# Performance work log

Measured on AMD Instinct MI355X. Metric: run time of the kernel, lower is better.

The kernel has to match this reference:

```python
import jax, jax.numpy as jnp
import numpy as np

DEPTH = 10
LEAF = 2 ** DEPTH          # 1024 leaves
NODE_NUM = 2 * LEAF - 1    # 2047
N = NODE_NUM + 1           # 2048 nodes incl. global node 0
ATTN = 4
D = 128
B = 8
L = 2


def _trace_children(ni):
    terms = []
    s, e = ni << 1, (ni << 1) | 1
    while s <= NODE_NUM and e <= NODE_NUM:
        terms.extend(range(s, e + 1))
        s <<= 1
        e = (e << 1) | 1
    return terms


def _trace_left(si):
    ni, cd, terms, stop = si + LEAF, DEPTH, [], False
    while not stop:
        cs = ni - ATTN + 1 - ((ni - ATTN + 1) & 1)
        stop = cs < 2 ** cd
        cs = max(2 ** cd, cs)
        terms.extend(range(cs, ni + 1))
        ni = (cs - 1) >> 1
        cd -= 1
    return terms


def _trace_right(ei):
    ni, cd, terms, stop = ei + LEAF, DEPTH, [], False
    while not stop:
        ce = ni + ATTN - 1 + ((ni - ATTN) & 1)
        stop = ce >= 2 ** (cd + 1)
        ce = min(2 ** (cd + 1) - 1, ce)
        terms.extend(range(ni, ce + 1))
        ni = (ce + 1) >> 1
        cd -= 1
    return terms


def _build_edges():
    src, dst = [], []
    for ni in range(1, NODE_NUM + 1):
        if ni < LEAF:
            t = _trace_children(ni)
        else:
            t = _trace_left(ni - LEAF) + _trace_right(ni - LEAF)
        src.extend(t)
        dst.extend([ni] * len(t))
    e = np.stack([np.asarray(src, np.int64), np.asarray(dst, np.int64)])  # [2, E]
    off = np.arange(B, dtype=np.int64) * N
    eb = (e[:, None, :] + off[None, :, None]).reshape(2, -1)  # batch-offset like _fetch_edge_data
    return eb.astype(np.int32)


def setup_inputs() -> dict:
    key = jax.random.key(0)
    k0, k1, k2 = jax.random.split(key, 3)
    s = 1.0 / np.sqrt(D)
    return {
        "elements": jax.random.normal(k0, (B, LEAF, D), jnp.float32),
        "ln_gamma": jnp.ones((L, D), jnp.float32),
        "ln_beta": jnp.zeros((L, D), jnp.float32),
        "w_nei": (jax.random.normal(k1, (L, D, D), jnp.float32) * s),
        "b_nei": jnp.zeros((L, D), jnp.float32),
        "w_root": (jax.random.normal(k2, (L, D, D), jnp.float32) * s),
        "edge_index": jnp.asarray(_build_edges()),
    }


def _sinusoid(pos, d):
    # ArbitraryPositionEncoder: sinusoidal encoding over (possibly negative) positions
    half = d // 2
    inv = jnp.exp(-jnp.arange(half, dtype=jnp.float32) * (np.log(10000.0) / half))
    ang = pos[:, None] * inv[None, :]  # [n, half]
    return jnp.stack([jnp.sin(ang), jnp.cos(ang)], -1).reshape(pos.shape[0], d)


def reference(elements, ln_gamma, ln_beta, w_nei, b_nei, w_root, edge_index):
    Bx, leaf, d = elements.shape
    depth = int(np.log2(leaf))
    # bottom-up tree compression (mean of two children)
    cur = elements
    levels = [cur]
    for _ in range(depth):
        cur = 0.5 * (cur[:, 0::2] + cur[:, 1::2])
        levels.append(cur)
    # node ordering: [global node 0 (=-1), root (level 0), ..., leaves (level depth)]
    node_feat = jnp.concatenate(
        [jnp.full((Bx, 1, d), -1.0, elements.dtype)] + levels[::-1], axis=1)  # [B, N, D]
    n = node_feat.shape[1]
    # positional encoding: vertical = floor(log2(idx)), horizontal = idx - 2^vertical
    idx = jnp.arange(n, dtype=jnp.float32)
    vpos = jnp.floor(jnp.log2(jnp.where(idx == 0, 0.5, idx)))
    hpos = idx - jnp.exp2(vpos)
    enc = jnp.concatenate([_sinusoid(hpos, d // 2), _sinusoid(vpos, d // 2)], -1)  # [N, D]
    x = (node_feat + enc[None]).reshape(Bx * n, d)
    src, dst = edge_index[0], edge_index[1]
    nseg = Bx * n
    deg = jnp.maximum(
        jax.ops.segment_sum(jnp.ones(src.shape, jnp.float32), dst, num_segments=nseg), 1.0)
    # DeepGCNLayer res+ blocks with SAGEConv (mean aggr)
    for l in range(ln_gamma.shape[0]):
        mu = jnp.mean(x, -1, keepdims=True)
        var = jnp.mean((x - mu) ** 2, -1, keepdims=True)
        h = (x - mu) * jax.lax.rsqrt(var + 1e-5) * ln_gamma[l] + ln_beta[l]
        h = jax.nn.gelu(h, approximate=False)
        agg = jax.ops.segment_sum(h[src], dst, num_segments=nseg) / deg[:, None]
        h = agg @ w_nei[l] + b_nei[l] + h @ w_root[l]
        x = x + h
    return x.reshape(Bx, n, d)
```

## Files before the change

kernel.cpp:

```cpp
#include <hip/hip_runtime.h>
#include <hip/hip_bf16.h>

#define LEAFN 1024
#define NN    2048
#define BATCH 8
#define DD    128
#define ROWS  (BATCH*NN)
#define AHS   384
#define NB    256
#define NT    1024

#define LOG1E4_OVER_32 0.28782313662425575f

#define SLACK 9
#define CSTRIDE 136
#define SB_OFF   0
#define SBT      520
#define S_OFF    33280
#define SSTR     232
#define DEG_OFF  48128
#define FB_OFF   48256
#define AGGL_OFF 54672
#define RED_OFF  63376
#define RED2_OFF 64400

typedef __bf16 bf16x8 __attribute__((ext_vector_type(8)));
typedef float  floatx4 __attribute__((ext_vector_type(4)));
typedef float  floatx2 __attribute__((ext_vector_type(2)));

__device__ __forceinline__ float bf2f(unsigned short u) {
  return __uint_as_float(((unsigned)u) << 16);
}
__device__ __forceinline__ unsigned short f2bf(float f) {
  unsigned u = __float_as_uint(f);
  u += 0x7FFFu + ((u >> 16) & 1u);
  return (unsigned short)(u >> 16);
}
__device__ __forceinline__ float gelu(float v) {
  return 0.5f * v * (1.0f + erff(v * 0.70710678118f));
}
__device__ __forceinline__ floatx2 bfpair(unsigned u) {
  floatx2 r;
  r[0] = __uint_as_float(u << 16);
  r[1] = __uint_as_float(u & 0xffff0000u);
  return r;
}

__device__ __forceinline__ float enc_val(int node, int d) {
  float hp, vp;
  if (node == 0) { hp = -0.5f; vp = -1.0f; }
  else {
    int v = 31 - __clz(node);
    hp = (float)(node - (1 << v));
    vp = (float)v;
  }
  float pos = (d < 64) ? hp : vp;
  int i = ((d < 64) ? d : (d - 64)) >> 1;
  float inv = __expf(-(float)i * LOG1E4_OVER_32);
  float ang = pos * inv;
  return (d & 1) ? __cosf(ang) : __sinf(ang);
}

__device__ __forceinline__ void win_cd(int jb, int cd, int& lo_, int& wd_) {
  int g0 = 1024 + jb * 32, g1 = g0 + 31;
  int a0 = g0 >> (10 - cd), a1 = g1 >> (10 - cd);
  int l = a0 - SLACK, h = a1 + SLACK;
  int lvlo = 1 << cd, lvhi = (2 << cd) - 1;
  lo_ = l < lvlo ? lvlo : l;
  int hh = h > lvhi ? lvhi : h;
  int w = hh - lo_ + 1;
  wd_ = w < 0 ? 0 : w;
}

__device__ __forceinline__ void gbarN(int* bar, int slot) {
  __syncthreads();
  if (threadIdx.x == 0) {
    int g = blockIdx.x & 7;
    int* base = bar + (slot * 8 + g) * 64;
    __threadfence();
    if (__hip_atomic_fetch_add(base, 1, __ATOMIC_RELAXED,
                               __HIP_MEMORY_SCOPE_AGENT) == 31)
      __hip_atomic_store(base + 32, 1, __ATOMIC_RELAXED,
                         __HIP_MEMORY_SCOPE_AGENT);
    while (!__hip_atomic_load(base + 32, __ATOMIC_RELAXED,
                              __HIP_MEMORY_SCOPE_AGENT))
      __builtin_amdgcn_s_sleep(1);
    __threadfence();
  }
  __syncthreads();
}

__device__ __forceinline__ void ph_tree(char* smemc, int b, int s,
                                        const float* __restrict__ elements,
                                        float* __restrict__ x,
                                        float* __restrict__ lvl4,
                                        unsigned short* __restrict__ ah,
                                        const float* __restrict__ gamma,
                                        const float* __restrict__ beta,
                                        float* __restrict__ sroot,
                                        float* xci, int* bar) {
  float* sm = (float*)smemc;
  floatx4* smv = (floatx4*)smemc;
  int tid = threadIdx.x;
  const float4* src = (const float4*)(elements + (size_t)(b * LEAFN + s * 64) * DD);
  for (int i = tid; i < 2048; i += NT) {
    int f = i * 4;
    int j = f >> 7, d = f & 127;
    *(float4*)&sm[(63 + j) * DD + d] = src[i];
  }
  __syncthreads();
  for (int lv = 5; lv >= 0; --lv) {
    int nodes = 1 << lv;
    for (int idx = tid; idx < nodes * 32; idx += NT) {
      int k = nodes + (idx >> 5);
      int j = idx & 31;
      smv[(k - 1) * 32 + j] = 0.5f * (smv[(2 * k - 1) * 32 + j] + smv[(2 * k) * 32 + j]);
    }
    __syncthreads();
  }
  if (tid < 32) ((floatx4*)&lvl4[(size_t)(b * 16 + s) * DD])[tid] = smv[tid];
  __syncthreads();
  if (tid == 0) {
    __threadfence();
    __hip_atomic_store(bar + 1536 + b * 64 + s * 4, 1, __ATOMIC_RELAXED,
                       __HIP_MEMORY_SCOPE_AGENT);
  }
  {
    int d2 = tid & 63;
    int i = d2 & 31;
    float inv = __expf(-(float)i * LOG1E4_OVER_32);
    bool lowhalf = d2 < 32;
    for (int idx2 = tid; idx2 < 127 * 64; idx2 += NT) {
      int row = idx2 >> 6;
      int k = row + 1;
      int lv = 31 - __clz(k);
      int g = ((16 + s) << lv) | (k - (1 << lv));
      float vp = (float)(lv + 4);
      float hp = (float)(g - (16 << lv));
      float pos = lowhalf ? hp : vp;
      float sv, cv;
      __sincosf(pos * inv, &sv, &cv);
      int base = row * DD + 2 * d2;
      float xv0 = sm[base] + sv;
      float xv1 = sm[base + 1] + cv;
      sm[base] = xv0; sm[base + 1] = xv1;
      if (k >= 64 || k <= 32) {
        float2 o = make_float2(xv0, xv1);
        *(float2*)&x[((size_t)(b * NN + g)) * DD + 2 * d2] = o;
      }
    }
  }
  __syncthreads();
  {
    int wave = tid >> 6, lane = tid & 63;
    if (wave >= 8) {
      int wl = wave & 7;
      int mt = wl >> 2, nq = wl & 3;
      int m = lane & 15, q = lane >> 4;
#pragma unroll
      for (int ci = 0; ci < 2; ++ci)
#pragma unroll
        for (int r = 0; r < 4; ++r) {
          int t = 32 + mt * 16 + q * 4 + r;
          int k = (t == 63) ? 1 : t + 1;
          int d = (nq * 2 + ci) * 16 + m;
          xci[ci * 4 + r] = sm[(k - 1) * DD + d];
        }
    }
  }
  __syncthreads();
  {
    int sub = tid & 7, dp = sub * 16;
    for (int rr = tid >> 3; rr < 127; rr += NT / 8) {
      float* rowp = &sm[rr * DD + dp];
      float4 q0 = *(float4*)rowp;
      float4 q1 = *(float4*)(rowp + 4);
      float4 q2 = *(float4*)(rowp + 8);
      float4 q3 = *(float4*)(rowp + 12);
      float v[16] = {q0.x, q0.y, q0.z, q0.w, q1.x, q1.y, q1.z, q1.w,
                     q2.x, q2.y, q2.z, q2.w, q3.x, q3.y, q3.z, q3.w};
      float s1 = 0.f, s2 = 0.f;
#pragma unroll
      for (int j = 0; j < 16; ++j) { s1 += v[j]; s2 += v[j] * v[j]; }
      s1 += __shfl_xor(s1, 1); s2 += __shfl_xor(s2, 1);
      s1 += __shfl_xor(s1, 2); s2 += __shfl_xor(s2, 2);
      s1 += __shfl_xor(s1, 4); s2 += __shfl_xor(s2, 4);
      float mu = s1 * (1.0f / 128.0f);
      float var = s2 * (1.0f / 128.0f) - mu * mu;
      float rinv = rsqrtf(var + 1e-5f);
      int k = rr + 1, lv = 31 - __clz(k);
      int g = ((16 + s) << lv) | (k - (1 << lv));
      __attribute__((aligned(16))) unsigned short o[16];
      float hv[16];
#pragma unroll
      for (int j = 0; j < 16; ++j) {
        hv[j] = gelu((v[j] - mu) * rinv * gamma[dp + j] + beta[dp + j]);
        o[j] = f2bf(hv[j]);
      }
      *(float4*)rowp        = make_float4(hv[0], hv[1], hv[2], hv[3]);
      *(float4*)(rowp + 4)  = make_float4(hv[4], hv[5], hv[6], hv[7]);
      *(float4*)(rowp + 8)  = make_float4(hv[8], hv[9], hv[10], hv[11]);
      *(float4*)(rowp + 12) = make_float4(hv[12], hv[13], hv[14], hv[15]);
      unsigned short* dst = &ah[(size_t)(b * NN + g) * AHS + 128 + dp];
      *(uint4*)&dst[0] = *(uint4*)&o[0];
      *(uint4*)&dst[8] = *(uint4*)&o[8];
    }
  }
  __syncthreads();
  for (int lv = 5; lv >= 0; --lv) {
    int nk = 1 << lv;
    float inv = 1.0f / (float)((1 << (7 - lv)) - 2);
    for (int idx = tid; idx < nk * 32; idx += NT) {
      int k = nk + (idx >> 5);
      int j = idx & 31;
      floatx4 S = smv[(2 * k - 1) * 32 + j] + smv[(2 * k) * 32 + j];
      if (lv < 5) S = S + smv[(4 * k - 1) * 32 + j] + smv[(4 * k + 1) * 32 + j];
      smv[(2 * k - 1) * 32 + j] = S;
      int g = ((16 + s) << lv) | (k - nk);
      ushort4 o;
      o.x = f2bf(S[0] * inv); o.y = f2bf(S[1] * inv);
      o.z = f2bf(S[2] * inv); o.w = f2bf(S[3] * inv);
      *(ushort4*)&ah[(size_t)(b * NN + g) * AHS + j * 4] = o;
    }
    __syncthreads();
  }
  if (tid < 32)
    ((floatx4*)&sroot[(size_t)(b * 16 + s) * DD])[tid] = smv[32 + tid];
}

__device__ __forceinline__ void ph_top(char* smemc, int b,
                                       const float* __restrict__ lvl4,
                                       unsigned short* __restrict__ ah,
                                       const float* __restrict__ gamma,
                                       const float* __restrict__ beta) {
  float (*xs)[DD] = (float(*)[DD])smemc;
  int tid = threadIdx.x;
  if (tid < 128) {
    int d = tid;
    float v[16];
    for (int j = 0; j < 16; ++j) v[j] = lvl4[(b * 16 + j) * DD + d];
    for (int j = 0; j < 8; ++j) v[j] = 0.5f * (v[2 * j] + v[2 * j + 1]);
    for (int j = 0; j < 8; ++j) xs[8 + j][d] = v[j] + enc_val(8 + j, d);
    for (int j = 0; j < 4; ++j) v[j] = 0.5f * (v[2 * j] + v[2 * j + 1]);
    for (int j = 0; j < 4; ++j) xs[4 + j][d] = v[j] + enc_val(4 + j, d);
    for (int j = 0; j < 2; ++j) v[j] = 0.5f * (v[2 * j] + v[2 * j + 1]);
    for (int j = 0; j < 2; ++j) xs[2 + j][d] = v[j] + enc_val(2 + j, d);
    v[0] = 0.5f * (v[0] + v[1]);
    xs[1][d] = v[0] + enc_val(1, d);
    xs[0][d] = -1.0f + enc_val(0, d);
  }
  __syncthreads();
  if (tid < 128) {
    int rr = tid >> 3, sub = tid & 7, dp = sub * 16;
    float w[16], s1 = 0.f, s2 = 0.f;
#pragma unroll
    for (int j = 0; j < 16; ++j) { w[j] = xs[rr][dp + j]; s1 += w[j]; s2 += w[j] * w[j]; }
    s1 += __shfl_xor(s1, 1); s2 += __shfl_xor(s2, 1);
    s1 += __shfl_xor(s1, 2); s2 += __shfl_xor(s2, 2);
    s1 += __shfl_xor(s1, 4); s2 += __shfl_xor(s2, 4);
    float mu = s1 * (1.0f / 128.0f);
    float var = s2 * (1.0f / 128.0f) - mu * mu;
    float rinv = rsqrtf(var + 1e-5f);
    __attribute__((aligned(16))) unsigned short o[16];
#pragma unroll
    for (int j = 0; j < 16; ++j)
      o[j] = f2bf(gelu((w[j] - mu) * rinv * gamma[dp + j] + beta[dp + j]));
    unsigned short* dst = &ah[(size_t)(b * NN + rr) * AHS + 128 + dp];
    *(uint4*)&dst[0] = *(uint4*)&o[0];
    *(uint4*)&dst[8] = *(uint4*)&o[8];
  }
  __syncthreads();
}

__device__ __forceinline__ void ph_aggsub(char* smemc, int b, int s,
                                          unsigned short* ah,
                                          float* __restrict__ sroot) {
  floatx4 (*S)[32] = (floatx4(*)[32])smemc;
  int tid = threadIdx.x;
  for (int idx = tid; idx < 32 * 32; idx += NT) {
    int k = 32 + (idx >> 5), q = idx & 31;
    int c = (16 + s) * 64 + (2 * k - 64);
    size_t a0 = (size_t)(b * NN + c) * AHS + 256 + q * 4;
    ushort4 u0 = *(const ushort4*)&ah[a0];
    ushort4 u1 = *(const ushort4*)&ah[a0 + AHS];
    floatx4 v;
    v[0] = bf2f(u0.x) + bf2f(u1.x);
    v[1] = bf2f(u0.y) + bf2f(u1.y);
    v[2] = bf2f(u0.z) + bf2f(u1.z);
    v[3] = bf2f(u0.w) + bf2f(u1.w);
    S[k][q] = v;
    int g = (16 + s) * 32 + (k - 32);
    int r = b * NN + g;
    ushort4 o;
    o.x = f2bf(v[0] * 0.5f); o.y = f2bf(v[1] * 0.5f);
    o.z = f2bf(v[2] * 0.5f); o.w = f2bf(v[3] * 0.5f);
    *(ushort4*)&ah[(size_t)r * AHS + q * 4] = o;
  }
  __syncthreads();
  for (int lv = 4; lv >= 0; --lv) {
    int nk = 1 << lv;
    float inv = 1.0f / (float)((1 << (7 - lv)) - 2);
    for (int idx = tid; idx < nk * 32; idx += NT) {
      int k = nk + (idx >> 5), q = idx & 31;
      int c = ((16 + s) << (lv + 1)) | (2 * k - 2 * nk);
      size_t a0 = (size_t)(b * NN + c) * AHS + 256 + q * 4;
      ushort4 u0 = *(const ushort4*)&ah[a0];
      ushort4 u1 = *(const ushort4*)&ah[a0 + AHS];
      floatx4 sc0 = S[2 * k][q], sc1 = S[2 * k + 1][q];
      floatx4 v;
      v[0] = bf2f(u0.x) + bf2f(u1.x) + sc0[0] + sc1[0];
      v[1] = bf2f(u0.y) + bf2f(u1.y) + sc0[1] + sc1[1];
      v[2] = bf2f(u0.z) + bf2f(u1.z) + sc0[2] + sc1[2];
      v[3] = bf2f(u0.w) + bf2f(u1.w) + sc0[3] + sc1[3];
      S[k][q] = v;
      int g = ((16 + s) << lv) | (k - nk);
      int r = b * NN + g;
      ushort4 o;
      o.x = f2bf(v[0] * inv); o.y = f2bf(v[1] * inv);
      o.z = f2bf(v[2] * inv); o.w = f2bf(v[3] * inv);
      *(ushort4*)&ah[(size_t)r * AHS + q * 4] = o;
    }
    __syncthreads();
  }
  for (int q = tid; q < 32; q += NT)
    ((floatx4*)sroot)[(size_t)(b * 16 + s) * 32 + q] = S[1][q];
}

__device__ __forceinline__ void ph_leafagg(char* smemc, int b, int jb,
                                           const int* __restrict__ srcv,
                                           const int* __restrict__ dstv,
                                           const int* __restrict__ s0a,
                                           const int* __restrict__ s1a,
                                           const unsigned short* __restrict__ eoff,
                                           unsigned short* ah, int hoff) {
  int tid = threadIdx.x;
  int lane = tid & 63, wv = tid >> 6;
  unsigned short* SB = (unsigned short*)(smemc + SB_OFF);
  unsigned short* S  = (unsigned short*)(smemc + S_OFF);
  float* invdeg = (float*)(smemc + DEG_OFF);
  unsigned int* fb = (unsigned int*)(smemc + FB_OFF);
  unsigned short* aggl = (unsigned short*)(smemc + AGGL_OFF);
  int rbase = b * NN + 1024 + jb * 32;

  int lo[11], wd[11], off[11];
  int acc_off = 0;
#pragma unroll
  for (int cd = 10; cd >= 1; --cd) {
    win_cd(jb, cd, lo[cd], wd[cd]);
    off[cd] = acc_off;
    acc_off += wd[cd];
  }

  for (int t = tid; t < 48128 / 16; t += NT)
    ((uint4*)smemc)[t] = make_uint4(0, 0, 0, 0);
  if (tid < 32)
    invdeg[tid] = 1.0f / (float)max(s1a[rbase + tid] - s0a[rbase + tid], 1);
  if (tid == 0) *fb = 0u;
  __syncthreads();

  {
    int E0 = s0a[rbase], E1 = s1a[rbase + 31];
    for (int e = E0 + tid; e < E1; e += NT) {
      int leaf = dstv[e] - rbase;
      unsigned kr = eoff[e];
      if (kr == 0xFFFFu) atomicOr(fb, 1u << leaf);
      else S[leaf * SSTR + kr] = 0x3F80;
    }
  }
#pragma unroll
  for (int cd = 10; cd >= 1; --cd) {
    int w = wd[cd];
    for (int t = tid; t < w * 16; t += NT) {
      int row = t >> 4, seg = t & 15;
      int kr = off[cd] + row;
      if (kr >= 128) continue;
      uint4 u = *(const uint4*)&ah[(size_t)(b * NN + lo[cd] + row) * AHS + hoff + seg * 8];
      int krl = kr;
      unsigned short* p = SB + ((krl >> 5) * 8 + (seg >> 1)) * SBT +
                          ((krl & 31) >> 3) * 128 + (seg & 1) * 64 + (krl & 7);
      p[0]  = (unsigned short)(u.x & 0xffff);
      p[8]  = (unsigned short)(u.x >> 16);
      p[16] = (unsigned short)(u.y & 0xffff);
      p[24] = (unsigned short)(u.y >> 16);
      p[32] = (unsigned short)(u.z & 0xffff);
      p[40] = (unsigned short)(u.z >> 16);
      p[48] = (unsigned short)(u.w & 0xffff);
      p[56] = (unsigned short)(u.w >> 16);
    }
  }
  __syncthreads();

  int m = lane & 15, q = lane >> 4;
  int mt = wv >> 3, nt = wv & 7;
  floatx4 acc = (floatx4){0.f, 0.f, 0.f, 0.f};
#pragma unroll
  for (int kcl = 0; kcl < 4; ++kcl) {
    bf16x8 a0 = *(const bf16x8*)&S[(mt * 16 + m) * SSTR + kcl * 32 + q * 8];
    bf16x8 bb = *(const bf16x8*)&SB[(kcl * 8 + nt) * SBT + lane * 8];
    acc = __builtin_amdgcn_mfma_f32_16x16x32_bf16(a0, bb, acc, 0, 0, 0);
  }
  __syncthreads();

  for (int t = tid; t < 24 * SBT / 8; t += NT)
    ((uint4*)SB)[t] = make_uint4(0, 0, 0, 0);
  __syncthreads();

#pragma unroll
  for (int cd = 10; cd >= 1; --cd) {
    int w = wd[cd];
    for (int t = tid; t < w * 16; t += NT) {
      int row = t >> 4, seg = t & 15;
      int kr = off[cd] + row;
      if (kr < 128) continue;
      uint4 u = *(const uint4*)&ah[(size_t)(b * NN + lo[cd] + row) * AHS + hoff + seg * 8];
      int krl = kr - 128;
      unsigned short* p = SB + ((krl >> 5) * 8 + (seg >> 1)) * SBT +
                          ((krl & 31) >> 3) * 128 + (seg & 1) * 64 + (krl & 7);
      p[0]  = (unsigned short)(u.x & 0xffff);
      p[8]  = (unsigned short)(u.x >> 16);
      p[16] = (unsigned short)(u.y & 0xffff);
      p[24] = (unsigned short)(u.y >> 16);
      p[32] = (unsigned short)(u.z & 0xffff);
      p[40] = (unsigned short)(u.z >> 16);
      p[48] = (unsigned short)(u.w & 0xffff);
      p[56] = (unsigned short)(u.w >> 16);
    }
  }
  __syncthreads();

#pragma unroll
  for (int kcl = 0; kcl < 3; ++kcl) {
    bf16x8 a0 = *(const bf16x8*)&S[(mt * 16 + m) * SSTR + (4 + kcl) * 32 + q * 8];
    bf16x8 bb = *(const bf16x8*)&SB[(kcl * 8 + nt) * SBT + lane * 8];
    acc = __builtin_amdgcn_mfma_f32_16x16x32_bf16(a0, bb, acc, 0, 0, 0);
  }
#pragma unroll
  for (int r = 0; r < 4; ++r) {
    int leaf = mt * 16 + q * 4 + r;
    aggl[leaf * CSTRIDE + nt * 16 + m] = f2bf(acc[r] * invdeg[leaf]);
  }
  __syncthreads();

  unsigned fbm = *fb;
  if (fbm && tid < 512) {
    int leaf = tid >> 4, c = tid & 15;
    if ((fbm >> leaf) & 1) {
      int e0 = s0a[rbase + leaf], e1 = s1a[rbase + leaf];
      floatx2 a0 = {0.f, 0.f}, a1 = {0.f, 0.f}, a2 = {0.f, 0.f}, a3 = {0.f, 0.f};
      for (int e = e0; e < e1; ++e) {
        int g = srcv[e] - b * NN;
        uint4 u = *(const uint4*)&ah[(size_t)(b * NN + g) * AHS + hoff + c * 8];
        a0 += bfpair(u.x); a1 += bfpair(u.y); a2 += bfpair(u.z); a3 += bfpair(u.w);
      }
      float inv = 1.0f / (float)max(e1 - e0, 1);
      __attribute__((aligned(16))) unsigned short o[8];
      o[0] = f2bf(a0[0] * inv); o[1] = f2bf(a0[1] * inv);
      o[2] = f2bf(a1[0] * inv); o[3] = f2bf(a1[1] * inv);
      o[4] = f2bf(a2[0] * inv); o[5] = f2bf(a2[1] * inv);
      o[6] = f2bf(a3[0] * inv); o[7] = f2bf(a3[1] * inv);
      *(uint4*)&aggl[leaf * CSTRIDE + c * 8] = *(uint4*)&o[0];
    }
  }
}

__device__ __forceinline__ void ph_topfin(int b,
                                          const float* __restrict__ sroot,
                                          unsigned short* ah, int hoff) {
  int d = threadIdx.x;
  float S16[16], h16[16], Sv[16];
#pragma unroll
  for (int j = 0; j < 16; ++j) S16[j] = sroot[(size_t)(b * 16 + j) * DD + d];
#pragma unroll
  for (int j = 0; j < 16; ++j)
    h16[j] = bf2f(ah[(size_t)(b * NN + 16 + j) * AHS + hoff + d]);
#pragma unroll
  for (int k = 8; k < 16; ++k)
    Sv[k] = h16[2 * k - 16] + h16[2 * k - 15] + S16[2 * k - 16] + S16[2 * k - 15];
#pragma unroll
  for (int k = 7; k >= 1; --k)
    Sv[k] = bf2f(ah[(size_t)(b * NN + 2 * k) * AHS + hoff + d]) +
            bf2f(ah[(size_t)(b * NN + 2 * k + 1) * AHS + hoff + d]) +
            Sv[2 * k] + Sv[2 * k + 1];
#pragma unroll
  for (int k = 1; k < 16; ++k) {
    int dv = 31 - __clz(k);
    float inv = 1.0f / (float)((1 << (11 - dv)) - 2);
    ah[(size_t)(b * NN + k) * AHS + d] = f2bf(Sv[k] * inv);
  }
  ah[(size_t)(b * NN) * AHS + d] = f2bf(0.0f);
}

__device__ __forceinline__ void ph_gemm32(char* redc, const unsigned short* aggl,
                                          int rowbase, unsigned short* ah,
                                          const unsigned short* __restrict__ wfl,
                                          const float* __restrict__ bn,
                                          float* __restrict__ x, int hoff_in,
                                          const float* __restrict__ gamma,
                                          const float* __restrict__ beta,
                                          float* xc, int first_layer) {
  int wave = threadIdx.x >> 6, lane = threadIdx.x & 63;
  bool act = wave < 8;
  int wl = wave & 7;
  int mt = wl >> 2, nq = wl & 3;
  int r0 = rowbase + mt * 16;
  int m = lane & 15, q = lane >> 4;
  floatx4 acc[2];
  acc[0] = (floatx4){0.f, 0.f, 0.f, 0.f};
  acc[1] = (floatx4){0.f, 0.f, 0.f, 0.f};
  if (act) {
    const unsigned short* arow = ah + (size_t)(r0 + m) * AHS + q * 8;
    const bf16x8* B = (const bf16x8*)wfl + lane;
#pragma unroll
    for (int kc = 0; kc < 8; ++kc) {
      bf16x8 a0;
      if (kc < 4)
        a0 = *(const bf16x8*)&aggl[(mt * 16 + m) * CSTRIDE + kc * 32 + q * 8];
      else
        a0 = *(const bf16x8*)(arow + hoff_in + (kc - 4) * 32);
#pragma unroll
      for (int ci = 0; ci < 2; ++ci) {
        bf16x8 bb = B[(kc * 8 + nq * 2 + ci) * 64];
        acc[ci] = __builtin_amdgcn_mfma_f32_16x16x32_bf16(a0, bb, acc[ci], 0, 0, 0);
      }
    }
  }
  if (first_layer) {
    float s1[4] = {0.f, 0.f, 0.f, 0.f}, s2[4] = {0.f, 0.f, 0.f, 0.f};
    if (act) {
#pragma unroll
      for (int ci = 0; ci < 2; ++ci) {
        int col = (nq * 2 + ci) * 16 + m;
        float bias = bn[col];
#pragma unroll
        for (int r = 0; r < 4; ++r) {
          int row = r0 + q * 4 + r;
          float v = x[(size_t)row * DD + col] + acc[ci][r] + bias;
          xc[ci * 4 + r] = v;
          s1[r] += v; s2[r] += v * v;
        }
      }
#pragma unroll
      for (int r = 0; r < 4; ++r) {
        s1[r] += __shfl_xor(s1[r], 1); s2[r] += __shfl_xor(s2[r], 1);
        s1[r] += __shfl_xor(s1[r], 2); s2[r] += __shfl_xor(s2[r], 2);
        s1[r] += __shfl_xor(s1[r], 4); s2[r] += __shfl_xor(s2[r], 4);
        s1[r] += __shfl_xor(s1[r], 8); s2[r] += __shfl_xor(s2[r], 8);
      }
    }
    float* red = (float*)redc;
    int rl = mt * 16 + q * 4;
    __syncthreads();
    if (act && m == 0) {
#pragma unroll
      for (int r = 0; r < 4; ++r) {
        red[(rl + r) * 4 + nq] = s1[r];
        red[128 + (rl + r) * 4 + nq] = s2[r];
      }
    }
    __syncthreads();
    if (act) {
      float mu[4], rv[4];
#pragma unroll
      for (int r = 0; r < 4; ++r) {
        float t1 = red[(rl + r) * 4] + red[(rl + r) * 4 + 1] +
                   red[(rl + r) * 4 + 2] + red[(rl + r) * 4 + 3];
        float t2 = red[128 + (rl + r) * 4] + red[128 + (rl + r) * 4 + 1] +
                   red[128 + (rl + r) * 4 + 2] + red[128 + (rl + r) * 4 + 3];
        mu[r] = t1 * (1.0f / 128.0f);
        float var = t2 * (1.0f / 128.0f) - mu[r] * mu[r];
        rv[r] = rsqrtf(var + 1e-5f);
      }
#pragma unroll
      for (int ci = 0; ci < 2; ++ci) {
        int col = (nq * 2 + ci) * 16 + m;
        float gm = gamma[col], bt = beta[col];
#pragma unroll
        for (int r = 0; r < 4; ++r) {
          int row = r0 + q * 4 + r;
          float hh = gelu((xc[ci * 4 + r] - mu[r]) * rv[r] * gm + bt);
          ah[(size_t)row * AHS + 256 + col] = f2bf(hh);
        }
      }
    }
  } else {
    if (act) {
#pragma unroll
      for (int ci = 0; ci < 2; ++ci) {
        int col = (nq * 2 + ci) * 16 + m;
        float bias = bn[col];
#pragma unroll
        for (int r = 0; r < 4; ++r) {
          int row = r0 + q * 4 + r;
          x[(size_t)row * DD + col] = xc[ci * 4 + r] + acc[ci][r] + bias;
        }
      }
    }
  }
}

// ... 125 lines not shown
  floatx4 acc = (floatx4){0.f, 0.f, 0.f, 0.f};
  int col = (ct & 7) * 16 + m;
  if (act) {
    const unsigned short* arow = ah + (size_t)(b * NN + m) * AHS + q * 8;
    const bf16x8* B = (const bf16x8*)wfl + lane;
#pragma unroll
    for (int kc = 0; kc < 8; ++kc) {
      int koff = (kc < 4) ? kc * 32 : hoff_in + (kc - 4) * 32;
      bf16x8 a0 = *(const bf16x8*)(arow + koff);
      bf16x8 bb = B[(kc * 8 + ct) * 64];
      acc = __builtin_amdgcn_mfma_f32_16x16x32_bf16(a0, bb, acc, 0, 0, 0);
    }
  }
  if (first_layer) {
    float s1[4] = {0.f, 0.f, 0.f, 0.f}, s2[4] = {0.f, 0.f, 0.f, 0.f};
    float bias = act ? bn[col] : 0.f;
    if (act) {
#pragma unroll
      for (int r = 0; r < 4; ++r) {
        float v = xc[r] + acc[r] + bias;
        xc[r] = v; s1[r] = v; s2[r] = v * v;
      }
#pragma unroll
      for (int r = 0; r < 4; ++r) {
        s1[r] += __shfl_xor(s1[r], 1); s2[r] += __shfl_xor(s2[r], 1);
        s1[r] += __shfl_xor(s1[r], 2); s2[r] += __shfl_xor(s2[r], 2);
        s1[r] += __shfl_xor(s1[r], 4); s2[r] += __shfl_xor(s2[r], 4);
        s1[r] += __shfl_xor(s1[r], 8); s2[r] += __shfl_xor(s2[r], 8);
      }
    }
    float* red = (float*)redc;
    __syncthreads();
    if (act && m == 0) {
#pragma unroll
      for (int r = 0; r < 4; ++r) {
        red[(q * 4 + r) * 8 + ct] = s1[r];
        red[128 + (q * 4 + r) * 8 + ct] = s2[r];
      }
    }
    __syncthreads();
    if (act) {
#pragma unroll
      for (int r = 0; r < 4; ++r) {
        float t1 = 0.f, t2 = 0.f;
#pragma unroll
        for (int j = 0; j < 8; ++j) {
          t1 += red[(q * 4 + r) * 8 + j];
          t2 += red[128 + (q * 4 + r) * 8 + j];
        }
        float mu = t1 * (1.0f / 128.0f);
        float var = t2 * (1.0f / 128.0f) - mu * mu;
        float rv = rsqrtf(var + 1e-5f);
        float hh = gelu((xc[r] - mu) * rv * gamma[col] + beta[col]);
        ah[(size_t)(b * NN + q * 4 + r) * AHS + 256 + col] = f2bf(hh);
      }
    }
  } else {
    if (act) {
      float bias = bn[col];
#pragma unroll
      for (int r = 0; r < 4; ++r)
        x[(size_t)(b * NN + q * 4 + r) * DD + col] = xc[r] + acc[r] + bias;
    }
  }
}

__global__ __launch_bounds__(NT, 1) void k_mega(
    const float* __restrict__ elements, const float* __restrict__ ln_gamma,
    const float* __restrict__ ln_beta, const float* __restrict__ w_nei,
    const float* __restrict__ b_nei, const float* __restrict__ w_root,
    const int* __restrict__ srcv, const int* __restrict__ dstv, int E,
    float* __restrict__ x, int* s0a, int* s1a, float* lvl4, float* sroot,
    unsigned short* wf, unsigned short* ah, unsigned short* eoff, int* bar) {
  __shared__ __align__(16) char smem[65536];
  int bid = blockIdx.x, tid = threadIdx.x;
  int b = bid & 7, gb = bid >> 3;
  int Eb = E >> 3;
  unsigned short* wfg = wf + (size_t)b * 65536;
  float xcl[8], xci[8], xct[4];
  int wv = tid >> 6;

  if (gb < 16) {
    ph_tree(smem, b, gb, elements, x, lvl4, ah, ln_gamma, ln_beta, sroot, xci, bar);
  } else if (gb < 24) {
    int base = b * Eb;
    for (int i = base + (gb - 16) * NT + tid; i < base + Eb; i += 8 * NT) {
      int dv = dstv[i];
      if (i == 0 || dstv[i - 1] != dv) s0a[dv] = i;
      if (i == base + Eb - 1 || dstv[i + 1] != dv) s1a[dv] = i + 1;
    }
    for (int i = base + (gb - 16) * NT + tid; i < base + Eb; i += 8 * NT) {
      int dl = dstv[i] - b * NN - 1024;
      unsigned short ov = 0xFFFFu;
      if (dl >= 0) {
        int jb2 = dl >> 5;
        int g = srcv[i] - b * NN;
        int lv = 31 - __clz(g);
        int acc2 = 0;
#pragma unroll
        for (int cd = 10; cd >= 1; --cd) {
          int lo_, wd_;
          win_cd(jb2, cd, lo_, wd_);
          if (cd == lv) {
            int idx = g - lo_;
            if ((unsigned)idx < (unsigned)wd_)
              ov = (unsigned short)(acc2 + idx);
          }
          acc2 += wd_;
        }
      }
      eoff[i] = ov;
    }
  } else if (gb < 28) {
    int gi = (gb - 24) * NT + tid;
    int lane = gi & 63, ct = (gi >> 6) & 7, kc = gi >> 9;
    int n = ct * 16 + (lane & 15);
    int k = kc * 32 + (lane >> 4) * 8;
    int kk = k & 127;
#pragma unroll
    for (int l = 0; l < 2; ++l) {
      const float* w = (k < 128) ? (w_nei + (size_t)l * DD * DD)
                                 : (w_root + (size_t)l * DD * DD);
      unsigned short* o = wfg + (size_t)l * 32768 + (size_t)gi * 8;
#pragma unroll
      for (int j = 0; j < 8; ++j) o[j] = f2bf(w[(size_t)(kk + j) * DD + n]);
    }
  } else if (gb == 28) {
    if (tid < 16) {
      while (!__hip_atomic_load(bar + 1536 + b * 64 + tid * 4, __ATOMIC_RELAXED,
                                __HIP_MEMORY_SCOPE_AGENT))
        __builtin_amdgcn_s_sleep(1);
      __threadfence();
    }
    __syncthreads();
    ph_top(smem, b, lvl4, ah, ln_gamma, ln_beta);
    {
      int ln = tid & 63, m_ = ln & 15, q_ = ln >> 4;
      if (wv < 8) {
        float (*xs)[DD] = (float(*)[DD])smem;
#pragma unroll
        for (int r = 0; r < 4; ++r) xct[r] = xs[q_ * 4 + r][wv * 16 + m_];
      }
    }
  }
  gbarN(bar, 0);

  if (gb == 28) {
    if (tid < 128) ph_topfin(b, sroot, ah, 128);
    __syncthreads();
    ph_gemm16t(smem + RED_OFF, b, ah, wfg, b_nei, x, 128,
               ln_gamma + DD, ln_beta + DD, xct, 1);
    __syncthreads();
  }
  ph_leafagg(smem, b, gb, srcv, dstv, s0a, s1a, eoff, ah, 128);
  __syncthreads();
  if (wv < 8) {
    ph_gemm32(smem + RED_OFF, (const unsigned short*)(smem + AGGL_OFF),
              b * NN + 1024 + gb * 32, ah, wfg, b_nei, x, 128,
              ln_gamma + DD, ln_beta + DD, xcl, 1);
  } else if (gb < 16) {
    ph_gemm32s(smem + RED2_OFF, b, gb, 32, ah, wfg, b_nei, x, 128,
               ln_gamma + DD, ln_beta + DD, xci, 1, nullptr);
  } else {
    ph_gemm32s(smem + RED2_OFF, b, gb - 16, 0, ah, wfg, b_nei, x, 128,
               ln_gamma + DD, ln_beta + DD, xci, 1, x);
  }
  gbarN(bar, 1);

  if (gb < 16) {
    ph_aggsub(smem, b, gb, ah, sroot);
    __syncthreads();
    if (tid == 0) {
      __threadfence();
      __hip_atomic_store(bar + 1024 + b * 64 + gb * 4, 1, __ATOMIC_RELAXED,
                         __HIP_MEMORY_SCOPE_AGENT);
    }
  }
  ph_leafagg(smem, b, gb, srcv, dstv, s0a, s1a, eoff, ah, 256);
  if (gb >= 16 && tid == 0) {
    while (!__hip_atomic_load(bar + 1024 + b * 64 + (gb - 16) * 4, __ATOMIC_RELAXED,
                              __HIP_MEMORY_SCOPE_AGENT))
      __builtin_amdgcn_s_sleep(1);
    __threadfence();
  }
  __syncthreads();
  if (wv < 8) {
    ph_gemm32(smem + RED_OFF, (const unsigned short*)(smem + AGGL_OFF),
              b * NN + 1024 + gb * 32, ah, wfg + 32768, b_nei + DD,
              x, 256, ln_gamma, ln_beta, xcl, 0);
  } else if (gb < 16) {
    ph_gemm32s(smem + RED2_OFF, b, gb, 32, ah, wfg + 32768, b_nei + DD, x, 256,
               ln_gamma, ln_beta, xci, 0, nullptr);
  } else {
    ph_gemm32s(smem + RED2_OFF, b, gb - 16, 0, ah, wfg + 32768, b_nei + DD, x, 256,
               ln_gamma, ln_beta, xci, 0, nullptr);
  }
  if (gb == 28) {
    if (tid < 16) {
      while (!__hip_atomic_load(bar + 1024 + b * 64 + tid * 4, __ATOMIC_RELAXED,
                                __HIP_MEMORY_SCOPE_AGENT))
        __builtin_amdgcn_s_sleep(1);
      __threadfence();
    }
    __syncthreads();
    if (tid < 128) ph_topfin(b, sroot, ah, 256);
    __syncthreads();
    ph_gemm16t(smem + RED_OFF, b, ah, wfg + 32768, b_nei + DD, x, 256,
               ln_gamma, ln_beta, xct, 0);
  }
}

extern "C" void kernel_launch(void* const* d_in, const int* in_sizes, int n_in,
                              void* d_out, int out_size, void* d_ws, size_t ws_size,
                              hipStream_t stream) {
  const float* elements = (const float*)d_in[0];
  const float* ln_gamma = (const float*)d_in[1];
  const float* ln_beta  = (const float*)d_in[2];
  const float* w_nei    = (const float*)d_in[3];
  const float* b_nei    = (const float*)d_in[4];
  const float* w_root   = (const float*)d_in[5];
  const int*   edge     = (const int*)d_in[6];
  int E = in_sizes[6] / 2;
  const int* srcv = edge;
  const int* dstv = edge + E;
  float* x = (float*)d_out;

  char* ws = (char*)d_ws;
  int*            bar   = (int*)ws;
  int*            s0    = (int*)(ws + 65536);
  int*            s1    = (int*)(ws + 131072);
  float*          lvl4  = (float*)(ws + 196608);
  float*          sroot = (float*)(ws + 262144);
  unsigned short* wf    = (unsigned short*)(ws + 327680);
  unsigned short* ah    = (unsigned short*)(ws + 327680 + 1048576);
  unsigned short* eoff  = (unsigned short*)(ws + 327680 + 1048576 + 12582912);

  hipMemsetAsync(bar, 0, 8192, stream);
  k_mega<<<dim3(NB), dim3(NT), 0, stream>>>(
      elements, ln_gamma, ln_beta, w_nei, b_nei, w_root,
      srcv, dstv, E, x, s0, s1, lvl4, sroot, wf, ah, eoff, bar);
}
```

Baseline: 160.7 us.

## Fuse tree levels pairwise and pack leaf adjacency into bitmasks for single-pass MFMA

The tree pooling and the subtree aggregation loops now handle two levels per pass, which halves the number of block barriers. Leaf aggregation replaces the dense bf16 adjacency matrix with a bitmask that is expanded in registers into MFMA A operands. The full gather buffer (7 k-chunks) is loaded in one pass instead of two passes with re-zeroing, and the mask is built once and reused by the second layer. The cost is extra select instructions to expand the mask, and a shared-memory layout where aggl overlaps SB, so its correctness depends on the barriers placed between them.

```diff
diff --git a/kernel.cpp b/kernel.cpp
--- a/kernel.cpp
+++ b/kernel.cpp
@@ -16,13 +16,12 @@
 #define CSTRIDE 136
 #define SB_OFF   0
 #define SBT      520
-#define S_OFF    33280
-#define SSTR     232
-#define DEG_OFF  48128
-#define FB_OFF   48256
-#define AGGL_OFF 54672
-#define RED_OFF  63376
-#define RED2_OFF 64400
+#define MSK_OFF  58240
+#define DEG_OFF  59264
+#define FB_OFF   59392
+#define AGGL_OFF 0
+#define RED_OFF  61440
+#define RED2_OFF 62464
 
 typedef __bf16 bf16x8 __attribute__((ext_vector_type(8)));
 typedef float  floatx4 __attribute__((ext_vector_type(4)));
@@ -88,6 +87,14 @@
     __threadfence();
   }
   __syncthreads();
+}
+
+__device__ __forceinline__ void st_agg(unsigned short* ah, int b, int g, int j,
+                                       floatx4 S, float inv) {
+  ushort4 o;
+  o.x = f2bf(S[0] * inv); o.y = f2bf(S[1] * inv);
+  o.z = f2bf(S[2] * inv); o.w = f2bf(S[3] * inv);
+  *(ushort4*)&ah[(size_t)(b * NN + g) * AHS + j * 4] = o;
 }
 
 __device__ __forceinline__ void ph_tree(char* smemc, int b, int s,
@@ -109,16 +116,36 @@
     *(float4*)&sm[(63 + j) * DD + d] = src[i];
   }
   __syncthreads();
-  for (int lv = 5; lv >= 0; --lv) {
-    int nodes = 1 << lv;
-    for (int idx = tid; idx < nodes * 32; idx += NT) {
-      int k = nodes + (idx >> 5);
-      int j = idx & 31;
-      smv[(k - 1) * 32 + j] = 0.5f * (smv[(2 * k - 1) * 32 + j] + smv[(2 * k) * 32 + j]);
-    }
-    __syncthreads();
-  }
-  if (tid < 32) ((floatx4*)&lvl4[(size_t)(b * 16 + s) * DD])[tid] = smv[tid];
+  {
+    for (int idx = tid; idx < 16 * 32; idx += NT) {
+      int k = 16 + (idx >> 5), j = idx & 31;
+      floatx4 a = 0.5f * (smv[(4 * k - 1) * 32 + j] + smv[(4 * k) * 32 + j]);
+      floatx4 c = 0.5f * (smv[(4 * k + 1) * 32 + j] + smv[(4 * k + 2) * 32 + j]);
+      smv[(2 * k - 1) * 32 + j] = a;
+      smv[(2 * k) * 32 + j] = c;
+      smv[(k - 1) * 32 + j] = 0.5f * (a + c);
+    }
+    __syncthreads();
+    for (int idx = tid; idx < 4 * 32; idx += NT) {
+      int k = 4 + (idx >> 5), j = idx & 31;
+      floatx4 a = 0.5f * (smv[(4 * k - 1) * 32 + j] + smv[(4 * k) * 32 + j]);
+      floatx4 c = 0.5f * (smv[(4 * k + 1) * 32 + j] + smv[(4 * k + 2) * 32 + j]);
+      smv[(2 * k - 1) * 32 + j] = a;
+      smv[(2 * k) * 32 + j] = c;
+      smv[(k - 1) * 32 + j] = 0.5f * (a + c);
+    }
+    __syncthreads();
+    for (int idx = tid; idx < 32; idx += NT) {
+      int j = idx;
+      floatx4 a = 0.5f * (smv[3 * 32 + j] + smv[4 * 32 + j]);
+      floatx4 c = 0.5f * (smv[5 * 32 + j] + smv[6 * 32 + j]);
+      smv[1 * 32 + j] = a;
+      smv[2 * 32 + j] = c;
+      floatx4 r = 0.5f * (a + c);
+      smv[j] = r;
+      ((floatx4*)&lvl4[(size_t)(b * 16 + s) * DD])[j] = r;
+    }
+  }
   __syncthreads();
   if (tid == 0) {
     __threadfence();
@@ -207,25 +234,48 @@
     }
   }
   __syncthreads();
-  for (int lv = 5; lv >= 0; --lv) {
-    int nk = 1 << lv;
-    float inv = 1.0f / (float)((1 << (7 - lv)) - 2);
-    for (int idx = tid; idx < nk * 32; idx += NT) {
-      int k = nk + (idx >> 5);
-      int j = idx & 31;
-      floatx4 S = smv[(2 * k - 1) * 32 + j] + smv[(2 * k) * 32 + j];
-      if (lv < 5) S = S + smv[(4 * k - 1) * 32 + j] + smv[(4 * k + 1) * 32 + j];
-      smv[(2 * k - 1) * 32 + j] = S;
-      int g = ((16 + s) << lv) | (k - nk);
-      ushort4 o;
-      o.x = f2bf(S[0] * inv); o.y = f2bf(S[1] * inv);
-      o.z = f2bf(S[2] * inv); o.w = f2bf(S[3] * inv);
-      *(ushort4*)&ah[(size_t)(b * NN + g) * AHS + j * 4] = o;
-    }
-    __syncthreads();
-  }
-  if (tid < 32)
-    ((floatx4*)&sroot[(size_t)(b * 16 + s) * DD])[tid] = smv[32 + tid];
+  {
+    for (int idx = tid; idx < 16 * 32; idx += NT) {
+      int k = 16 + (idx >> 5), j = idx & 31;
+      floatx4 sa = smv[(4 * k - 1) * 32 + j] + smv[(4 * k) * 32 + j];
+      floatx4 sc = smv[(4 * k + 1) * 32 + j] + smv[(4 * k + 2) * 32 + j];
+      floatx4 sk = (smv[(2 * k - 1) * 32 + j] + smv[(2 * k) * 32 + j]) + (sa + sc);
+      smv[(4 * k - 1) * 32 + j] = sa;
+      smv[(4 * k + 1) * 32 + j] = sc;
+      smv[(2 * k - 1) * 32 + j] = sk;
+      st_agg(ah, b, ((16 + s) << 5) | (2 * k - 32), j, sa, 0.5f);
+      st_agg(ah, b, ((16 + s) << 5) | (2 * k + 1 - 32), j, sc, 0.5f);
+      st_agg(ah, b, ((16 + s) << 4) | (k - 16), j, sk, 1.0f / 6.0f);
+    }
+    __syncthreads();
+    for (int idx = tid; idx < 4 * 32; idx += NT) {
+      int k = 4 + (idx >> 5), j = idx & 31;
+      floatx4 sa = (smv[(4 * k - 1) * 32 + j] + smv[(4 * k) * 32 + j]) +
+                   (smv[(8 * k - 1) * 32 + j] + smv[(8 * k + 1) * 32 + j]);
+      floatx4 sc = (smv[(4 * k + 1) * 32 + j] + smv[(4 * k + 2) * 32 + j]) +
+                   (smv[(8 * k + 3) * 32 + j] + smv[(8 * k + 5) * 32 + j]);
+      floatx4 sk = (smv[(2 * k - 1) * 32 + j] + smv[(2 * k) * 32 + j]) + (sa + sc);
+      smv[(4 * k - 1) * 32 + j] = sa;
+      smv[(4 * k + 1) * 32 + j] = sc;
+      smv[(2 * k - 1) * 32 + j] = sk;
+      st_agg(ah, b, ((16 + s) << 3) | (2 * k - 8), j, sa, 1.0f / 14.0f);
+      st_agg(ah, b, ((16 + s) << 3) | (2 * k + 1 - 8), j, sc, 1.0f / 14.0f);
+      st_agg(ah, b, ((16 + s) << 2) | (k - 4), j, sk, 1.0f / 30.0f);
+    }
+    __syncthreads();
+    for (int idx = tid; idx < 32; idx += NT) {
+      int j = idx;
+      floatx4 sa = (smv[3 * 32 + j] + smv[4 * 32 + j]) +
+                   (smv[7 * 32 + j] + smv[9 * 32 + j]);
+      floatx4 sc = (smv[5 * 32 + j] + smv[6 * 32 + j]) +
+                   (smv[11 * 32 + j] + smv[13 * 32 + j]);
+      floatx4 sk = (smv[1 * 32 + j] + smv[2 * 32 + j]) + (sa + sc);
+      st_agg(ah, b, ((16 + s) << 1) | 0, j, sa, 1.0f / 62.0f);
+      st_agg(ah, b, ((16 + s) << 1) | 1, j, sc, 1.0f / 62.0f);
+      st_agg(ah, b, (16 + s), j, sk, 1.0f / 126.0f);
+      ((floatx4*)&sroot[(size_t)(b * 16 + s) * DD])[j] = sk;
+    }
+  }
 }
 
 __device__ __forceinline__ void ph_top(char* smemc, int b,
@@ -289,41 +339,87 @@
     v[2] = bf2f(u0.z) + bf2f(u1.z);
     v[3] = bf2f(u0.w) + bf2f(u1.w);
     S[k][q] = v;
-    int g = (16 + s) * 32 + (k - 32);
-    int r = b * NN + g;
-    ushort4 o;
-    o.x = f2bf(v[0] * 0.5f); o.y = f2bf(v[1] * 0.5f);
-    o.z = f2bf(v[2] * 0.5f); o.w = f2bf(v[3] * 0.5f);
-    *(ushort4*)&ah[(size_t)r * AHS + q * 4] = o;
-  }
-  __syncthreads();
-  for (int lv = 4; lv >= 0; --lv) {
-    int nk = 1 << lv;
-    float inv = 1.0f / (float)((1 << (7 - lv)) - 2);
-    for (int idx = tid; idx < nk * 32; idx += NT) {
-      int k = nk + (idx >> 5), q = idx & 31;
-      int c = ((16 + s) << (lv + 1)) | (2 * k - 2 * nk);
-      size_t a0 = (size_t)(b * NN + c) * AHS + 256 + q * 4;
-      ushort4 u0 = *(const ushort4*)&ah[a0];
-      ushort4 u1 = *(const ushort4*)&ah[a0 + AHS];
-      floatx4 sc0 = S[2 * k][q], sc1 = S[2 * k + 1][q];
-      floatx4 v;
-      v[0] = bf2f(u0.x) + bf2f(u1.x) + sc0[0] + sc1[0];
-      v[1] = bf2f(u0.y) + bf2f(u1.y) + sc0[1] + sc1[1];
-      v[2] = bf2f(u0.z) + bf2f(u1.z) + sc0[2] + sc1[2];
-      v[3] = bf2f(u0.w) + bf2f(u1.w) + sc0[3] + sc1[3];
-      S[k][q] = v;
-      int g = ((16 + s) << lv) | (k - nk);
-      int r = b * NN + g;
-      ushort4 o;
-      o.x = f2bf(v[0] * inv); o.y = f2bf(v[1] * inv);
-      o.z = f2bf(v[2] * inv); o.w = f2bf(v[3] * inv);
-      *(ushort4*)&ah[(size_t)r * AHS + q * 4] = o;
-    }
-    __syncthreads();
-  }
-  for (int q = tid; q < 32; q += NT)
-    ((floatx4*)sroot)[(size_t)(b * 16 + s) * 32 + q] = S[1][q];
+    st_agg(ah, b, (16 + s) * 32 + (k - 32), q, v, 0.5f);
+  }
+  __syncthreads();
+  for (int idx = tid; idx < 8 * 32; idx += NT) {
+    int k = 8 + (idx >> 5), q = idx & 31;
+    size_t aa = (size_t)(b * NN + (((16 + s) << 5) | (4 * k - 32))) * AHS + 256 + q * 4;
+    ushort4 u0 = *(const ushort4*)&ah[aa];
+    ushort4 u1 = *(const ushort4*)&ah[aa + AHS];
+    size_t ab = (size_t)(b * NN + (((16 + s) << 5) | (4 * k + 2 - 32))) * AHS + 256 + q * 4;
+    ushort4 w0 = *(const ushort4*)&ah[ab];
+    ushort4 w1 = *(const ushort4*)&ah[ab + AHS];
+    size_t ac = (size_t)(b * NN + (((16 + s) << 4) | (2 * k - 16))) * AHS + 256 + q * 4;
+    ushort4 h0 = *(const ushort4*)&ah[ac];
+    ushort4 h1 = *(const ushort4*)&ah[ac + AHS];
+    floatx4 s4a, s4b, s3;
+    floatx4 sc0 = S[4 * k][q], sc1 = S[4 * k + 1][q];
+    floatx4 sd0 = S[4 * k + 2][q], sd1 = S[4 * k + 3][q];
+    s4a[0] = bf2f(u0.x) + bf2f(u1.x) + sc0[0] + sc1[0];
+    s4a[1] = bf2f(u0.y) + bf2f(u1.y) + sc0[1] + sc1[1];
+    s4a[2] = bf2f(u0.z) + bf2f(u1.z) + sc0[2] + sc1[2];
+    s4a[3] = bf2f(u0.w) + bf2f(u1.w) + sc0[3] + sc1[3];
+    s4b[0] = bf2f(w0.x) + bf2f(w1.x) + sd0[0] + sd1[0];
+    s4b[1] = bf2f(w0.y) + bf2f(w1.y) + sd0[1] + sd1[1];
+    s4b[2] = bf2f(w0.z) + bf2f(w1.z) + sd0[2] + sd1[2];
+    s4b[3] = bf2f(w0.w) + bf2f(w1.w) + sd0[3] + sd1[3];
+    s3[0] = bf2f(h0.x) + bf2f(h1.x) + s4a[0] + s4b[0];
+    s3[1] = bf2f(h0.y) + bf2f(h1.y) + s4a[1] + s4b[1];
+    s3[2] = bf2f(h0.z) + bf2f(h1.z) + s4a[2] + s4b[2];
+    s3[3] = bf2f(h0.w) + bf2f(h1.w) + s4a[3] + s4b[3];
+    S[2 * k][q] = s4a; S[2 * k + 1][q] = s4b; S[k][q] = s3;
+    st_agg(ah, b, ((16 + s) << 4) | (2 * k - 16), q, s4a, 1.0f / 6.0f);
+    st_agg(ah, b, ((16 + s) << 4) | (2 * k + 1 - 16), q, s4b, 1.0f / 6.0f);
+    st_agg(ah, b, ((16 + s) << 3) | (k - 8), q, s3, 1.0f / 14.0f);
+  }
+  __syncthreads();
+  for (int idx = tid; idx < 2 * 32; idx += NT) {
+    int k = 2 + (idx >> 5), q = idx & 31;
+    size_t aa = (size_t)(b * NN + (((16 + s) << 3) | (4 * k - 8))) * AHS + 256 + q * 4;
+    ushort4 u0 = *(const ushort4*)&ah[aa];
+    ushort4 u1 = *(const ushort4*)&ah[aa + AHS];
+    size_t ab = (size_t)(b * NN + (((16 + s) << 3) | (4 * k + 2 - 8))) * AHS + 256 + q * 4;
+    ushort4 w0 = *(const ushort4*)&ah[ab];
+    ushort4 w1 = *(const ushort4*)&ah[ab + AHS];
+    size_t ac = (size_t)(b * NN + (((16 + s) << 2) | (2 * k - 4))) * AHS + 256 + q * 4;
+    ushort4 h0 = *(const ushort4*)&ah[ac];
+    ushort4 h1 = *(const ushort4*)&ah[ac + AHS];
+    floatx4 s2a, s2b, s1v;
+    floatx4 sc0 = S[4 * k][q], sc1 = S[4 * k + 1][q];
+    floatx4 sd0 = S[4 * k + 2][q], sd1 = S[4 * k + 3][q];
+    s2a[0] = bf2f(u0.x) + bf2f(u1.x) + sc0[0] + sc1[0];
+    s2a[1] = bf2f(u0.y) + bf2f(u1.y) + sc0[1] + sc1[1];
+    s2a[2] = bf2f(u0.z) + bf2f(u1.z) + sc0[2] + sc1[2];
+    s2a[3] = bf2f(u0.w) + bf2f(u1.w) + sc0[3] + sc1[3];
+    s2b[0] = bf2f(w0.x) + bf2f(w1.x) + sd0[0] + sd1[0];
+    s2b[1] = bf2f(w0.y) + bf2f(w1.y) + sd0[1] + sd1[1];
+    s2b[2] = bf2f(w0.z) + bf2f(w1.z) + sd0[2] + sd1[2];
+    s2b[3] = bf2f(w0.w) + bf2f(w1.w) + sd0[3] + sd1[3];
+    s1v[0] = bf2f(h0.x) + bf2f(h1.x) + s2a[0] + s2b[0];
+    s1v[1] = bf2f(h0.y) + bf2f(h1.y) + s2a[1] + s2b[1];
+    s1v[2] = bf2f(h0.z) + bf2f(h1.z) + s2a[2] + s2b[2];
+    s1v[3] = bf2f(h0.w) + bf2f(h1.w) + s2a[3] + s2b[3];
+    S[2 * k][q] = s2a; S[2 * k + 1][q] = s2b; S[k][q] = s1v;
+    st_agg(ah, b, ((16 + s) << 2) | (2 * k - 4), q, s2a, 1.0f / 30.0f);
+    st_agg(ah, b, ((16 + s) << 2) | (2 * k + 1 - 4), q, s2b, 1.0f / 30.0f);
+    st_agg(ah, b, ((16 + s) << 1) | (k - 2), q, s1v, 1.0f / 62.0f);
+  }
+  __syncthreads();
+  for (int idx = tid; idx < 32; idx += NT) {
+    int q = idx;
+    size_t aa = (size_t)(b * NN + (((16 + s) << 1) | 0)) * AHS + 256 + q * 4;
+    ushort4 u0 = *(const ushort4*)&ah[aa];
+    ushort4 u1 = *(const ushort4*)&ah[aa + AHS];
+    floatx4 sc0 = S[2][q], sc1 = S[3][q];
+    floatx4 s0v;
+    s0v[0] = bf2f(u0.x) + bf2f(u1.x) + sc0[0] + sc1[0];
+    s0v[1] = bf2f(u0.y) + bf2f(u1.y) + sc0[1] + sc1[1];
+    s0v[2] = bf2f(u0.z) + bf2f(u1.z) + sc0[2] + sc1[2];
+    s0v[3] = bf2f(u0.w) + bf2f(u1.w) + sc0[3] + sc1[3];
+    st_agg(ah, b, (16 + s), q, s0v, 1.0f / 126.0f);
+    ((floatx4*)sroot)[(size_t)(b * 16 + s) * 32 + q] = s0v;
+  }
 }
 
 __device__ __forceinline__ void ph_leafagg(char* smemc, int b, int jb,
@@ -332,11 +428,12 @@
                                            const int* __restrict__ s0a,
                                            const int* __restrict__ s1a,
                                            const unsigned short* __restrict__ eoff,
-                                           unsigned short* ah, int hoff) {
+                                           unsigned short* ah, int hoff,
+                                           int build) {
   int tid = threadIdx.x;
   int lane = tid & 63, wv = tid >> 6;
   unsigned short* SB = (unsigned short*)(smemc + SB_OFF);
-  unsigned short* S  = (unsigned short*)(smemc + S_OFF);
+  unsigned* msk = (unsigned*)(smemc + MSK_OFF);
   float* invdeg = (float*)(smemc + DEG_OFF);
   unsigned int* fb = (unsigned int*)(smemc + FB_OFF);
   unsigned short* aggl = (unsigned short*)(smemc + AGGL_OFF);
@@ -351,20 +448,24 @@
     acc_off += wd[cd];
   }
 
-  for (int t = tid; t < 48128 / 16; t += NT)
+  for (int t = tid; t < 3640; t += NT)
     ((uint4*)smemc)[t] = make_uint4(0, 0, 0, 0);
-  if (tid < 32)
-    invdeg[tid] = 1.0f / (float)max(s1a[rbase + tid] - s0a[rbase + tid], 1);
-  if (tid == 0) *fb = 0u;
-  __syncthreads();
-
-  {
+  if (build) {
+    if (tid < 256) msk[tid] = 0u;
+    if (tid >= 256 && tid < 288)
+      invdeg[tid - 256] = 1.0f /
+          (float)max(s1a[rbase + tid - 256] - s0a[rbase + tid - 256], 1);
+    if (tid == 288) *fb = 0u;
+  }
+  __syncthreads();
+
+  if (build) {
     int E0 = s0a[rbase], E1 = s1a[rbase + 31];
     for (int e = E0 + tid; e < E1; e += NT) {
       int leaf = dstv[e] - rbase;
       unsigned kr = eoff[e];
       if (kr == 0xFFFFu) atomicOr(fb, 1u << leaf);
-      else S[leaf * SSTR + kr] = 0x3F80;
+      else atomicOr(&msk[leaf * 8 + (kr >> 5)], 1u << (kr & 31));
     }
   }
 #pragma unroll
@@ -373,11 +474,9 @@
     for (int t = tid; t < w * 16; t += NT) {
       int row = t >> 4, seg = t & 15;
       int kr = off[cd] + row;
-      if (kr >= 128) continue;
       uint4 u = *(const uint4*)&ah[(size_t)(b * NN + lo[cd] + row) * AHS + hoff + seg * 8];
-      int krl = kr;
-      unsigned short* p = SB + ((krl >> 5) * 8 + (seg >> 1)) * SBT +
-                          ((krl & 31) >> 3) * 128 + (seg & 1) * 64 + (krl & 7);
+      unsigned short* p = SB + ((kr >> 5) * 8 + (seg >> 1)) * SBT +
+                          ((kr & 31) >> 3) * 128 + (seg & 1) * 64 + (kr & 7);
       p[0]  = (unsigned short)(u.x & 0xffff);
       p[8]  = (unsigned short)(u.x >> 16);
       p[16] = (unsigned short)(u.y & 0xffff);
@@ -392,59 +491,32 @@
 
   int m = lane & 15, q = lane >> 4;
   int mt = wv >> 3, nt = wv & 7;
+  int arow = mt * 16 + m;
   floatx4 acc = (floatx4){0.f, 0.f, 0.f, 0.f};
 #pragma unroll
-  for (int kcl = 0; kcl < 4; ++kcl) {
-    bf16x8 a0 = *(const bf16x8*)&S[(mt * 16 + m) * SSTR + kcl * 32 + q * 8];
+  for (int kcl = 0; kcl < 7; ++kcl) {
+    unsigned mw = msk[arow * 8 + kcl];
+    unsigned bits = (mw >> (q * 8)) & 0xffu;
+    union { uint4 u; bf16x8 v; } A;
+    A.u.x = ((bits & 1u)  ? 0x3F80u : 0u) | ((bits & 2u)   ? 0x3F800000u : 0u);
+    A.u.y = ((bits & 4u)  ? 0x3F80u : 0u) | ((bits & 8u)   ? 0x3F800000u : 0u);
+    A.u.z = ((bits & 16u) ? 0x3F80u : 0u) | ((bits & 32u)  ? 0x3F800000u : 0u);
+    A.u.w = ((bits & 64u) ? 0x3F80u : 0u) | ((bits & 128u) ? 0x3F800000u : 0u);
     bf16x8 bb = *(const bf16x8*)&SB[(kcl * 8 + nt) * SBT + lane * 8];
-    acc = __builtin_amdgcn_mfma_f32_16x16x32_bf16(a0, bb, acc, 0, 0, 0);
-  }
-  __syncthreads();
-
-  for (int t = tid; t < 24 * SBT / 8; t += NT)
-    ((uint4*)SB)[t] = make_uint4(0, 0, 0, 0);
-  __syncthreads();
-
-#pragma unroll
-  for (int cd = 10; cd >= 1; --cd) {
-    int w = wd[cd];
-    for (int t = tid; t < w * 16; t += NT) {
-      int row = t >> 4, seg = t & 15;
-      int kr = off[cd] + row;
-      if (kr < 128) continue;
-      uint4 u = *(const uint4*)&ah[(size_t)(b * NN + lo[cd] + row) * AHS + hoff + seg * 8];
-      int krl = kr - 128;
-      unsigned short* p = SB + ((krl >> 5) * 8 + (seg >> 1)) * SBT +
-                          ((krl & 31) >> 3) * 128 + (seg & 1) * 64 + (krl & 7);
-      p[0]  = (unsigned short)(u.x & 0xffff);
-      p[8]  = (unsigned short)(u.x >> 16);
-      p[16] = (unsigned short)(u.y & 0xffff);
-      p[24] = (unsigned short)(u.y >> 16);
-      p[32] = (unsigned short)(u.z & 0xffff);
-      p[40] = (unsigned short)(u.z >> 16);
-      p[48] = (unsigned short)(u.w & 0xffff);
-      p[56] = (unsigned short)(u.w >> 16);
-    }
-  }
-  __syncthreads();
-
-#pragma unroll
-  for (int kcl = 0; kcl < 3; ++kcl) {
-    bf16x8 a0 = *(const bf16x8*)&S[(mt * 16 + m) * SSTR + (4 + kcl) * 32 + q * 8];
-    bf16x8 bb = *(const bf16x8*)&SB[(kcl * 8 + nt) * SBT + lane * 8];
-    acc = __builtin_amdgcn_mfma_f32_16x16x32_bf16(a0, bb, acc, 0, 0, 0);
-  }
+    acc = __builtin_amdgcn_mfma_f32_16x16x32_bf16(A.v, bb, acc, 0, 0, 0);
+  }
+  __syncthreads();
+
+  unsigned fbm = *fb;
 #pragma unroll
   for (int r = 0; r < 4; ++r) {
     int leaf = mt * 16 + q * 4 + r;
-    aggl[leaf * CSTRIDE + nt * 16 + m] = f2bf(acc[r] * invdeg[leaf]);
-  }
-  __syncthreads();
-
-  unsigned fbm = *fb;
+    if (!((fbm >> leaf) & 1u))
+      aggl[leaf * CSTRIDE + nt * 16 + m] = f2bf(acc[r] * invdeg[leaf]);
+  }
   if (fbm && tid < 512) {
     int leaf = tid >> 4, c = tid & 15;
-    if ((fbm >> leaf) & 1) {
+    if ((fbm >> leaf) & 1u) {
       int e0 = s0a[rbase + leaf], e1 = s1a[rbase + leaf];
       floatx2 a0 = {0.f, 0.f}, a1 = {0.f, 0.f}, a2 = {0.f, 0.f}, a3 = {0.f, 0.f};
       for (int e = e0; e < e1; ++e) {
@@ -876,7 +948,7 @@
                ln_gamma + DD, ln_beta + DD, xct, 1);
     __syncthreads();
   }
-  ph_leafagg(smem, b, gb, srcv, dstv, s0a, s1a, eoff, ah, 128);
+  ph_leafagg(smem, b, gb, srcv, dstv, s0a, s1a, eoff, ah, 128, 1);
   __syncthreads();
   if (wv < 8) {
     ph_gemm32(smem + RED_OFF, (const unsigned short*)(smem + AGGL_OFF),
@@ -900,7 +972,7 @@
                          __HIP_MEMORY_SCOPE_AGENT);
     }
   }
-  ph_leafagg(smem, b, gb, srcv, dstv, s0a, s1a, eoff, ah, 256);
+  ph_leafagg(smem, b, gb, srcv, dstv, s0a, s1a, eoff, ah, 256, 0);
   if (gb >= 16 && tid == 0) {
     while (!__hip_atomic_load(bar + 1024 + b * 64 + (gb - 16) * 4, __ATOMIC_RELAXED,
                               __HIP_MEMORY_SCOPE_AGENT))
```

Result: no change. 158.1 us (median of 2 runs) (-1.7%).
